# Kernel tuning notes

Measured on AMD Instinct MI355X. Metric: run time of the kernel, lower is better.

The kernel has to match this reference:

```python
import jax, jax.numpy as jnp
import numpy as np

H = 16          # num_heads
DH = 128        # head_dim
TILE = 128      # tile_size
TOPK = 8        # top_k_tiles
NEG = -1e10


def _rotate_half(x):
    half = x.shape[-1] // 2
    return jnp.concatenate([-x[..., half:], x[..., :half]], axis=-1)


def setup_inputs() -> dict:
    key = jax.random.key(0)
    B, S, D = 2, 2048, H * DH
    ks = jax.random.split(key, 5)
    x = jax.random.normal(ks[0], (B, S, D), dtype=jnp.float32)
    scale = 0.02
    wq = jax.random.normal(ks[1], (D, H * DH), dtype=jnp.float32) * scale
    wk = jax.random.normal(ks[2], (D, H * DH), dtype=jnp.float32) * scale
    wv = jax.random.normal(ks[3], (D, H * DH), dtype=jnp.float32) * scale
    wo = jax.random.normal(ks[4], (H * DH, D), dtype=jnp.float32) * scale
    # RoPE tables: freqs_cis.real / .imag, shape [S, head_dim//2]
    inv_freq = 1.0 / (10000.0 ** (np.arange(0, DH, 2, dtype=np.float32) / DH))
    angles = np.arange(S, dtype=np.float32)[:, None] * inv_freq[None, :]
    cos = jnp.asarray(np.cos(angles), dtype=jnp.float32)
    sin = jnp.asarray(np.sin(angles), dtype=jnp.float32)
    return {"x": x, "wq": wq, "wk": wk, "wv": wv, "wo": wo, "cos": cos, "sin": sin}


def reference(x, wq, wk, wv, wo, cos, sin):
    B, S, D = x.shape
    # QKV projections -> [B, H, S, Dh]
    q = (x @ wq).reshape(B, S, H, DH).transpose(0, 2, 1, 3)
    k = (x @ wk).reshape(B, S, H, DH).transpose(0, 2, 1, 3)
    v = (x @ wv).reshape(B, S, H, DH).transpose(0, 2, 1, 3)
    # RoPE (half-split / rotate_half form), in fp32 as in source
    cf = jnp.concatenate([cos, cos], axis=-1)[None, None].astype(jnp.float32)  # [1,1,S,Dh]
    sf = jnp.concatenate([sin, sin], axis=-1)[None, None].astype(jnp.float32)
    q = q.astype(jnp.float32)
    k = k.astype(jnp.float32)
    q = q * cf + _rotate_half(q) * sf
    k = k * cf + _rotate_half(k) * sf
    # Full causal logits [B,H,S,S] (short-seq branch: seq_len <= 8192)
    scale = 1.0 / jnp.sqrt(jnp.float32(DH))
    logits = jnp.einsum('bhqd,bhkd->bhqk', q, k) * scale
    causal = jnp.tril(jnp.ones((S, S), dtype=bool))
    logits = jnp.where(causal[None, None], logits, NEG)
    # Tile scoring: softmax over representative rows, tile max-pool, top-k tiles
    num_tiles = S // TILE
    rep_pos = jnp.arange(TILE - 1, S, TILE)           # last query of each tile
    rep_w = jax.nn.softmax(logits[:, :, rep_pos, :], axis=-1)  # [B,H,nt,S]
    tile_scores = jnp.max(rep_w.reshape(B, H, num_tiles, num_tiles, TILE), axis=-1)
    _, group_tile_indices = jax.lax.top_k(tile_scores, min(TOPK, num_tiles))  # [B,H,nt,topk]
    # Full causal attention (explicit path, same math as dot_product_attention is_causal)
    weights = jax.nn.softmax(logits, axis=-1)
    out = jnp.einsum('bhqk,bhkd->bhqd', weights, v)
    out = out.transpose(0, 2, 1, 3).reshape(B, S, H * DH)
    out = out @ wo
    return out, group_tile_indices
```

## Files before the change

kernel.cpp:

```cpp
#include <hip/hip_runtime.h>
#include <cstdint>
#include <cstddef>


#define S_LEN 2048
#define NH 16
#define DHD 128
#define DMODEL 2048
#define MROWS 4096
#define SCALE 0.08838834764831845f
#define NEG10 -1e10f

typedef short short8 __attribute__((ext_vector_type(8)));
typedef __bf16 bf16x8 __attribute__((ext_vector_type(8)));
typedef float f32x4 __attribute__((ext_vector_type(4)));

#define MFMA16(a, b, c) __builtin_amdgcn_mfma_f32_16x16x32_bf16((a), (b), (c), 0, 0, 0)

__device__ __forceinline__ void gl16(const void* g, void* s) {
  __builtin_amdgcn_global_load_lds(
      (const __attribute__((address_space(1))) void*)g,
      (__attribute__((address_space(3))) void*)s, 16, 0, 0);
}

__device__ __forceinline__ unsigned short f2bf(float f) {
  unsigned u = __float_as_uint(f);
  return (unsigned short)((u + 0x7fffu + ((u >> 16) & 1u)) >> 16);
}
__device__ __forceinline__ float bf2f(unsigned short h) {
  return __uint_as_float(((unsigned)h) << 16);
}

__global__ __launch_bounds__(256) void k_split_x(const float* __restrict__ x,
                                                 unsigned short* __restrict__ xh,
                                                 unsigned short* __restrict__ xl, int n4) {
  int i = blockIdx.x * blockDim.x + threadIdx.x;
  for (; i < n4; i += gridDim.x * blockDim.x) {
    float4 v = ((const float4*)x)[i];
    float f[4] = {v.x, v.y, v.z, v.w};
    unsigned short hh[4], ll[4];
#pragma unroll
    for (int j = 0; j < 4; j++) {
      hh[j] = f2bf(f[j]);
      ll[j] = f2bf(f[j] - bf2f(hh[j]));
    }
    ((ushort4*)xh)[i] = make_ushort4(hh[0], hh[1], hh[2], hh[3]);
    ((ushort4*)xl)[i] = make_ushort4(ll[0], ll[1], ll[2], ll[3]);
  }
}

template <int LO>
__global__ __launch_bounds__(256) void k_transw(const float* __restrict__ w,
                                                unsigned short* __restrict__ th,
                                                unsigned short* __restrict__ tl) {
  int n = blockIdx.x * 256 + threadIdx.x;
  int r0 = blockIdx.y * 32;
  float vals[32];
#pragma unroll
  for (int j = 0; j < 32; j++) vals[j] = w[(size_t)(r0 + j) * DMODEL + n];
  unsigned short hs[32];
#pragma unroll
  for (int j = 0; j < 32; j++) hs[j] = f2bf(vals[j]);
  unsigned short* dsth = th + (size_t)n * DMODEL + r0;
#pragma unroll
  for (int c = 0; c < 4; c++) {
    short8 v;
#pragma unroll
    for (int j = 0; j < 8; j++) v[j] = (short)hs[c * 8 + j];
    *(short8*)(dsth + c * 8) = v;
  }
  if (LO) {
    unsigned short ls[32];
#pragma unroll
    for (int j = 0; j < 32; j++) ls[j] = f2bf(vals[j] - bf2f(hs[j]));
    unsigned short* dstl = tl + (size_t)n * DMODEL + r0;
#pragma unroll
    for (int c = 0; c < 4; c++) {
      short8 v;
#pragma unroll
      for (int j = 0; j < 8; j++) v[j] = (short)ls[c * 8 + j];
      *(short8*)(dstl + c * 8) = v;
    }
  }
}

template <int SPLIT, int EPI>
__global__ __launch_bounds__(256) void k_gemm(const unsigned short* __restrict__ A,
                                              const unsigned short* __restrict__ Al,
                                              const unsigned short* __restrict__ Bt,
                                              const unsigned short* __restrict__ Btl,
                                              void* __restrict__ outp) {
  constexpr int NSM = (SPLIT ? 4 : 2) * 4096;
  __shared__ unsigned short sm[NSM];
  unsigned short* sAh = sm;
  unsigned short* sAl = SPLIT ? (sm + 4096) : nullptr;
  unsigned short* sBh = sm + (SPLIT ? 8192 : 4096);
  unsigned short* sBl = SPLIT ? (sm + 12288) : nullptr;

  const int tid = threadIdx.x;
  const int l = tid & 63, w = tid >> 6;
  const int lr = l & 15, lk = l >> 4;
  const int rowBase = blockIdx.y * 128;
  const int colBase = blockIdx.x * 128;
  const int wr = (w >> 1) * 64, wc = (w & 1) * 64;

  f32x4 zero = {0.f, 0.f, 0.f, 0.f};
  f32x4 acc[4][4];
#pragma unroll
  for (int mi = 0; mi < 4; mi++)
#pragma unroll
    for (int ni = 0; ni < 4; ni++) acc[mi][ni] = zero;

  for (int kt = 0; kt < 64; ++kt) {
#pragma unroll
    for (int p = 0; p < 2; ++p) {
      int c = w * 128 + p * 64 + l;
      int row = c >> 2, sl = c & 3;
      int kbl = sl ^ ((row >> 1) & 3);
      size_t srca = (size_t)(rowBase + row) * DMODEL + kt * 32 + kbl * 8;
      gl16(A + srca, (char*)sAh + c * 16);
      if (SPLIT) gl16(Al + srca, (char*)sAl + c * 16);
      size_t srcb = (size_t)(colBase + row) * DMODEL + kt * 32 + kbl * 8;
      gl16(Bt + srcb, (char*)sBh + c * 16);
      if (SPLIT) gl16(Btl + srcb, (char*)sBl + c * 16);
    }
    __syncthreads();

    bf16x8 ah[4], alo[4], bh[4], blo[4];
#pragma unroll
    for (int mi = 0; mi < 4; mi++) {
      int row = wr + mi * 16 + lr;
      int off = row * 32 + ((lk ^ ((row >> 1) & 3)) * 8);
      ah[mi] = *(const bf16x8*)(sAh + off);
      if (SPLIT) alo[mi] = *(const bf16x8*)(sAl + off);
    }
#pragma unroll
    for (int ni = 0; ni < 4; ni++) {
      int row = wc + ni * 16 + lr;
      int off = row * 32 + ((lk ^ ((row >> 1) & 3)) * 8);
      bh[ni] = *(const bf16x8*)(sBh + off);
      if (SPLIT) blo[ni] = *(const bf16x8*)(sBl + off);
    }
#pragma unroll
    for (int mi = 0; mi < 4; mi++)
#pragma unroll
      for (int ni = 0; ni < 4; ni++) {
        acc[mi][ni] = MFMA16(ah[mi], bh[ni], acc[mi][ni]);
        if (SPLIT) {
          acc[mi][ni] = MFMA16(alo[mi], bh[ni], acc[mi][ni]);
          acc[mi][ni] = MFMA16(ah[mi], blo[ni], acc[mi][ni]);
        }
      }
    __syncthreads();
  }

#pragma unroll
  for (int mi = 0; mi < 4; mi++)
#pragma unroll
    for (int ni = 0; ni < 4; ni++)
#pragma unroll
      for (int r = 0; r < 4; r++) {
        int row = rowBase + wr + mi * 16 + lk * 4 + r;
        int col = colBase + wc + ni * 16 + lr;
        float v = acc[mi][ni][r];
        if (EPI == 2) {
          ((float*)outp)[(size_t)row * DMODEL + col] = v;
        } else {
          size_t idx = (((size_t)(row >> 11) * NH + (col >> 7)) * S_LEN + (row & 2047)) * DHD +
                       (col & 127);
          if (EPI == 1)
            ((float*)outp)[idx] = v;
          else
            ((unsigned short*)outp)[idx] = f2bf(v);
        }
      }
}

__global__ __launch_bounds__(256) void k_rope_q(unsigned short* __restrict__ q,
                                                const float* __restrict__ cosT,
                                                const float* __restrict__ sinT) {
  int t = blockIdx.x * blockDim.x + threadIdx.x;
  int row = t >> 4;
  int i4 = (t & 15) * 4;
  int s = row & 2047;
  unsigned short* p0 = q + (size_t)row * DHD + i4;
  unsigned short* p1 = p0 + 64;
  ushort4 a = *(ushort4*)p0, b = *(ushort4*)p1;
  float4 c = *(const float4*)(cosT + (size_t)s * 64 + i4);
  float4 sn = *(const float4*)(sinT + (size_t)s * 64 + i4);
  float av[4] = {bf2f(a.x), bf2f(a.y), bf2f(a.z), bf2f(a.w)};
  float bv[4] = {bf2f(b.x), bf2f(b.y), bf2f(b.z), bf2f(b.w)};
  float cv[4] = {c.x, c.y, c.z, c.w}, sv[4] = {sn.x, sn.y, sn.z, sn.w};
  unsigned short na[4], nb[4];
#pragma unroll
  for (int j = 0; j < 4; j++) {
    na[j] = f2bf(av[j] * cv[j] - bv[j] * sv[j]);
    nb[j] = f2bf(bv[j] * cv[j] + av[j] * sv[j]);
  }
  *(ushort4*)p0 = make_ushort4(na[0], na[1], na[2], na[3]);
  *(ushort4*)p1 = make_ushort4(nb[0], nb[1], nb[2], nb[3]);
}

__global__ __launch_bounds__(256) void k_rope_k(float* __restrict__ kf,
                                                unsigned short* __restrict__ kb,
                                                const float* __restrict__ cosT,
                                                const float* __restrict__ sinT) {
  int t = blockIdx.x * blockDim.x + threadIdx.x;
  int row = t >> 4;
  int i4 = (t & 15) * 4;
  int s = row & 2047;
  float* p0 = kf + (size_t)row * DHD + i4;
  float* p1 = p0 + 64;
  float4 a = *(float4*)p0, b = *(float4*)p1;
  float4 c = *(const float4*)(cosT + (size_t)s * 64 + i4);
  float4 sn = *(const float4*)(sinT + (size_t)s * 64 + i4);
  float av[4] = {a.x, a.y, a.z, a.w}, bv[4] = {b.x, b.y, b.z, b.w};
  float cv[4] = {c.x, c.y, c.z, c.w}, sv[4] = {sn.x, sn.y, sn.z, sn.w};
  float na[4], nb[4];
#pragma unroll
  for (int j = 0; j < 4; j++) {
    na[j] = av[j] * cv[j] - bv[j] * sv[j];
    nb[j] = bv[j] * cv[j] + av[j] * sv[j];
  }
  *(float4*)p0 = make_float4(na[0], na[1], na[2], na[3]);
  *(float4*)p1 = make_float4(nb[0], nb[1], nb[2], nb[3]);
  unsigned short* kb0 = kb + (size_t)row * DHD + i4;
  *(ushort4*)kb0 = make_ushort4(f2bf(na[0]), f2bf(na[1]), f2bf(na[2]), f2bf(na[3]));
  *(ushort4*)(kb0 + 64) = make_ushort4(f2bf(nb[0]), f2bf(nb[1]), f2bf(nb[2]), f2bf(nb[3]));
}

__global__ __launch_bounds__(256) void k_vtrans(const unsigned short* __restrict__ v,
                                                unsigned short* __restrict__ vt) {
  int bh = blockIdx.y;
  int s0 = blockIdx.x * 64 + (threadIdx.x >> 7) * 32;
  int d = threadIdx.x & 127;
  unsigned short tmp[32];
#pragma unroll
  for (int j = 0; j < 32; j++) tmp[j] = v[((size_t)bh * S_LEN + s0 + j) * DHD + d];
  unsigned short* dst = vt + ((size_t)bh * DHD + d) * S_LEN + s0;
#pragma unroll
  for (int c = 0; c < 4; c++) {
    short8 x;
#pragma unroll
    for (int j = 0; j < 8; j++) x[j] = (short)tmp[c * 8 + j];
    *(short8*)(dst + c * 8) = x;
  }
}

__global__ __launch_bounds__(256) void k_attn(const unsigned short* __restrict__ q,
                                              const unsigned short* __restrict__ k,
                                              const unsigned short* __restrict__ vt,
                                              unsigned short* __restrict__ o) {
  __shared__ unsigned short sK[64 * 128];
  __shared__ unsigned short sV[128 * 64];
  __shared__ unsigned short sP[128 * 72];
  const int qt = blockIdx.x, bh = blockIdx.y;
  const int b = bh >> 4, h = bh & 15;
  const int tid = threadIdx.x, l = tid & 63, w = tid >> 6;
  const int lr = l & 15, lk = l >> 4;
  const int q0 = qt * 128;
  const size_t kvbase = (size_t)bh * S_LEN * DHD;

  bf16x8 qf[2][4];
#pragma unroll
  for (int mi = 0; mi < 2; mi++)
#pragma unroll
    for (int kd = 0; kd < 4; kd++) {
      int row = q0 + w * 32 + mi * 16 + lr;
      qf[mi][kd] = *(const bf16x8*)(q + kvbase + (size_t)row * DHD + kd * 32 + lk * 8);
    }

  f32x4 zero = {0.f, 0.f, 0.f, 0.f};
  f32x4 acc[2][8];
#pragma unroll
  for (int mi = 0; mi < 2; mi++)
#pragma unroll
    for (int ni = 0; ni < 8; ni++) acc[mi][ni] = zero;
  float mrow[2][4], lsum[2][4];
#pragma unroll
  for (int mi = 0; mi < 2; mi++)
#pragma unroll
    for (int r = 0; r < 4; r++) {
      mrow[mi][r] = -3e38f;
      lsum[mi][r] = 0.f;
    }

  const int nkt = 2 * qt + 2;
  for (int kt = 0; kt < nkt; ++kt) {
#pragma unroll
    for (int p = 0; p < 4; ++p) {
      int c = p * 256 + w * 64 + l;
      int kp = c >> 4, sl = c & 15;
      int sls = sl ^ (kp & 7);
      gl16(k + kvbase + (size_t)(kt * 64 + kp) * DHD + sls * 8, (char*)sK + c * 16);
    }
#pragma unroll
    for (int p = 0; p < 4; ++p) {
      int c = p * 256 + w * 64 + l;
      int dh = c >> 3, sl = c & 7;
      int sls = sl ^ (dh & 7);
      gl16(vt + ((size_t)bh * DHD + dh) * S_LEN + kt * 64 + sls * 8, (char*)sV + c * 16);
    }
    __syncthreads();

    f32x4 sf[2][4];
#pragma unroll
    for (int mi = 0; mi < 2; mi++)
#pragma unroll
      for (int nk = 0; nk < 4; nk++) {
        f32x4 sacc = zero;
#pragma unroll
        for (int kd = 0; kd < 4; kd++) {
          int row = nk * 16 + lr;
          int off = row * 128 + (((kd * 4 + lk) ^ (row & 7)) * 8);
          bf16x8 kf = *(const bf16x8*)(sK + off);
          sacc = MFMA16(qf[mi][kd], kf, sacc);
        }
        sf[mi][nk] = sacc;
      }

#pragma unroll
    for (int mi = 0; mi < 2; mi++) {
#pragma unroll
      for (int r = 0; r < 4; r++) {
        int qpos = q0 + w * 32 + mi * 16 + lk * 4 + r;
        float lg[4];
        float mx = -3e38f;
#pragma unroll
        for (int nk = 0; nk < 4; nk++) {
          int kpos = kt * 64 + nk * 16 + lr;
          float vsc = sf[mi][nk][r] * SCALE;
          if (kpos > qpos) vsc = -3e38f;
          lg[nk] = vsc;
          mx = fmaxf(mx, vsc);
        }
#pragma unroll
        for (int d = 1; d < 16; d <<= 1) mx = fmaxf(mx, __shfl_xor(mx, d));
        float mnew = fmaxf(mrow[mi][r], mx);
        float corr = expf(mrow[mi][r] - mnew);
        float ps = 0.f;
        unsigned short pb[4];
#pragma unroll
        for (int nk = 0; nk < 4; nk++) {
          float p = expf(lg[nk] - mnew);
          ps += p;
          pb[nk] = f2bf(p);
        }
#pragma unroll
        for (int d = 1; d < 16; d <<= 1) ps += __shfl_xor(ps, d);
        lsum[mi][r] = lsum[mi][r] * corr + ps;
        mrow[mi][r] = mnew;
#pragma unroll
        for (int ni = 0; ni < 8; ni++) acc[mi][ni][r] *= corr;
        int prow = w * 32 + mi * 16 + lk * 4 + r;
#pragma unroll
        for (int nk = 0; nk < 4; nk++) sP[prow * 72 + nk * 16 + lr] = pb[nk];
      }
    }
    __syncthreads();

    bf16x8 pa[2][2];
#pragma unroll
    for (int mi = 0; mi < 2; mi++)
#pragma unroll
      for (int ks = 0; ks < 2; ks++) {
        int row = w * 32 + mi * 16 + lr;
        pa[mi][ks] = *(const bf16x8*)(sP + row * 72 + ks * 32 + lk * 8);
      }
#pragma unroll
    for (int ni = 0; ni < 8; ni++) {
#pragma unroll
      for (int ks = 0; ks < 2; ks++) {
        int row = ni * 16 + lr;
        int off = row * 64 + (((ks * 4 + lk) ^ (row & 7)) * 8);
        bf16x8 vf = *(const bf16x8*)(sV + off);
#pragma unroll
        for (int mi = 0; mi < 2; mi++) acc[mi][ni] = MFMA16(pa[mi][ks], vf, acc[mi][ni]);
      }
    }
    __syncthreads();
  }

#pragma unroll
  for (int mi = 0; mi < 2; mi++)
#pragma unroll
    for (int r = 0; r < 4; r++) {
      float inv = 1.0f / lsum[mi][r];
      int srow = q0 + w * 32 + mi * 16 + lk * 4 + r;
      size_t base = ((size_t)b * S_LEN + srow) * DMODEL + h * DHD;
#pragma unroll
      for (int ni = 0; ni < 8; ni++) o[base + ni * 16 + lr] = f2bf(acc[mi][ni][r] * inv);
    }
}

__global__ __launch_bounds__(256) void k_score(const float* __restrict__ x,
                                               const float* __restrict__ wq,
                                               const float* __restrict__ cosT,
                                               const float* __restrict__ sinT,
                                               const float* __restrict__ kf,
                                               float* __restrict__ idxout) {
  const int t = blockIdx.x, bh = blockIdx.y;
  const int b = bh >> 4, h = bh & 15;
  const int srep = t * 128 + 127;
  const int tid = threadIdx.x;
  __shared__ float qr[128];
  __shared__ float part[256];
  __shared__ unsigned keys[16];

  {
    const int dh = tid & 127, half = tid >> 7;
    const float* xrow = x + ((size_t)b * S_LEN + srep) * DMODEL;
    const float* wcol = wq + (size_t)h * DHD + dh;
    float s0 = 0.f, s1 = 0.f, s2 = 0.f, s3 = 0.f;
    const int dbase = half * 1024;
    for (int d = 0; d < 1024; d += 4) {
      int dd = dbase + d;
      s0 = fmaf(xrow[dd], wcol[(size_t)dd * DMODEL], s0);
      s1 = fmaf(xrow[dd + 1], wcol[(size_t)(dd + 1) * DMODEL], s1);
      s2 = fmaf(xrow[dd + 2], wcol[(size_t)(dd + 2) * DMODEL], s2);
      s3 = fmaf(xrow[dd + 3], wcol[(size_t)(dd + 3) * DMODEL], s3);
    }
    part[tid] = (s0 + s1) + (s2 + s3);
  }
  if (tid < 16) keys[tid] = ~__float_as_uint(NEG10);
  __syncthreads();
  if (tid < 64) {
    int i = tid;
    float q0v = part[i] + part[i + 128];
    float q1v = part[i + 64] + part[i + 192];
    float c = cosT[(size_t)srep * 64 + i], sn = sinT[(size_t)srep * 64 + i];
    qr[i] = q0v * c - q1v * sn;
    qr[i + 64] = q1v * c + q0v * sn;
  }
  __syncthreads();

  for (int j = tid; j <= srep; j += 256) {
    const float4* krow = (const float4*)(kf + ((size_t)bh * S_LEN + j) * DHD);
    float a0 = 0.f, a1 = 0.f, a2 = 0.f, a3 = 0.f;
#pragma unroll 8
    for (int d4 = 0; d4 < 32; d4++) {
      float4 kv = krow[d4];
      const float* qq = qr + d4 * 4;
      a0 = fmaf(kv.x, qq[0], a0);
      a1 = fmaf(kv.y, qq[1], a1);
      a2 = fmaf(kv.z, qq[2], a2);
      a3 = fmaf(kv.w, qq[3], a3);
    }
    float lg = ((a0 + a1) + (a2 + a3)) * SCALE;
    unsigned u = __float_as_uint(lg);
    unsigned key = (u & 0x80000000u) ? ~u : (u | 0x80000000u);
    atomicMax(&keys[j >> 7], key);
  }
  __syncthreads();

  if (tid == 0) {
    unsigned used = 0;
    float* dst = idxout + ((size_t)bh * 16 + t) * 8;
    for (int r = 0; r < 8; ++r) {
      int best = -1;
      unsigned bk = 0;
#pragma unroll
      for (int tl = 0; tl < 16; ++tl) {
        if (used & (1u << tl)) continue;
        unsigned kv = keys[tl];
        if (best < 0 || kv > bk) {
          bk = kv;
          best = tl;
        }
      }
      used |= (1u << best);
      dst[r] = (float)best;
    }
  }
}

extern "C" void kernel_launch(void* const* d_in, const int* in_sizes, int n_in,
                              void* d_out, int out_size, void* d_ws, size_t ws_size,
                              hipStream_t stream) {
  (void)in_sizes; (void)n_in; (void)out_size; (void)ws_size;
  const float* x = (const float*)d_in[0];
  const float* wq = (const float*)d_in[1];
  const float* wk = (const float*)d_in[2];
  const float* wv = (const float*)d_in[3];
  const float* wo = (const float*)d_in[4];
  const float* cosT = (const float*)d_in[5];
  const float* sinT = (const float*)d_in[6];
  float* out0 = (float*)d_out;
  float* out1 = out0 + (size_t)MROWS * DMODEL;
  float* kf32 = out0;

  char* ws = (char*)d_ws;
  size_t off = 0;
  auto alloc = [&](size_t bytes) {
    void* p = ws + off;
    off += (bytes + 255) & ~(size_t)255;
    return p;
  };
  unsigned short* xh = (unsigned short*)alloc(16777216);
  unsigned short* xl = (unsigned short*)alloc(16777216);
  unsigned short* wqT = (unsigned short*)alloc(8388608);
  unsigned short* wkT = (unsigned short*)alloc(8388608);
  unsigned short* wkTl = (unsigned short*)alloc(8388608);
  unsigned short* wvT = (unsigned short*)alloc(8388608);
  unsigned short* woT = (unsigned short*)alloc(8388608);
  unsigned short* qbf = (unsigned short*)alloc(16777216);
  unsigned short* kbf = (unsigned short*)alloc(16777216);
  unsigned short* vbf = (unsigned short*)alloc(16777216);
  unsigned short* obf = xh;
  unsigned short* vtbf = xl;

  k_split_x<<<2048, 256, 0, stream>>>(x, xh, xl, MROWS * DMODEL / 4);
  dim3 gtw(8, 64);
  k_transw<0><<<gtw, 256, 0, stream>>>(wq, wqT, nullptr);
  k_transw<1><<<gtw, 256, 0, stream>>>(wk, wkT, wkTl);
  k_transw<0><<<gtw, 256, 0, stream>>>(wv, wvT, nullptr);
  k_transw<0><<<gtw, 256, 0, stream>>>(wo, woT, nullptr);

  dim3 gg(16, 32);
  k_gemm<0, 0><<<gg, 256, 0, stream>>>(xh, nullptr, wqT, nullptr, qbf);
  k_gemm<1, 1><<<gg, 256, 0, stream>>>(xh, xl, wkT, wkTl, kf32);
  k_gemm<0, 0><<<gg, 256, 0, stream>>>(xh, nullptr, wvT, nullptr, vbf);

  k_rope_q<<<4096, 256, 0, stream>>>(qbf, cosT, sinT);
  k_rope_k<<<4096, 256, 0, stream>>>(kf32, kbf, cosT, sinT);

  k_vtrans<<<dim3(32, 32), 256, 0, stream>>>(vbf, vtbf);
  k_attn<<<dim3(16, 32), 256, 0, stream>>>(qbf, kbf, vtbf, obf);

  k_score<<<dim3(16, 32), 256, 0, stream>>>(x, wq, cosT, sinT, kf32, out1);

  k_gemm<0, 2><<<gg, 256, 0, stream>>>(obf, nullptr, woT, nullptr, out0);
}
```

Baseline: 781.6 us.

## Shrink attention query tile to 64 rows and use exp2 softmax

The attention kernel now gives each block 64 query rows instead of 128, so each wave handles 16 rows and the grid doubles to 32x32 blocks. Causal masking is applied only on the diagonal key tile, and the softmax folds log2(e) into the scale so it can use exp2f. The aim is more blocks and higher occupancy (launch bounds now request 3 blocks per CU) and less masking and exponent work. In exchange, each block reuses every K/V tile it loads across half as many queries, so total K/V traffic from global memory roughly doubles.

```diff
diff --git a/kernel.cpp b/kernel.cpp
--- a/kernel.cpp
+++ b/kernel.cpp
@@ -9,6 +9,7 @@
 #define DMODEL 2048
 #define MROWS 4096
 #define SCALE 0.08838834764831845f
+#define SCALE_L2E (0.08838834764831845f * 1.4426950408889634f)
 #define NEG10 -1e10f
 
 typedef short short8 __attribute__((ext_vector_type(8)));
@@ -247,126 +248,113 @@
   }
 }
 
-__global__ __launch_bounds__(256) void k_attn(const unsigned short* __restrict__ q,
-                                              const unsigned short* __restrict__ k,
-                                              const unsigned short* __restrict__ vt,
-                                              unsigned short* __restrict__ o) {
+__global__ __launch_bounds__(256, 3) void k_attn(const unsigned short* __restrict__ q,
+                                                 const unsigned short* __restrict__ k,
+                                                 const unsigned short* __restrict__ vt,
+                                                 unsigned short* __restrict__ o) {
   __shared__ unsigned short sK[64 * 128];
   __shared__ unsigned short sV[128 * 64];
-  __shared__ unsigned short sP[128 * 72];
+  __shared__ unsigned short sP[64 * 72];
   const int qt = blockIdx.x, bh = blockIdx.y;
   const int b = bh >> 4, h = bh & 15;
   const int tid = threadIdx.x, l = tid & 63, w = tid >> 6;
   const int lr = l & 15, lk = l >> 4;
-  const int q0 = qt * 128;
+  const int q0 = qt * 64;
   const size_t kvbase = (size_t)bh * S_LEN * DHD;
 
-  bf16x8 qf[2][4];
-#pragma unroll
-  for (int mi = 0; mi < 2; mi++)
-#pragma unroll
-    for (int kd = 0; kd < 4; kd++) {
-      int row = q0 + w * 32 + mi * 16 + lr;
-      qf[mi][kd] = *(const bf16x8*)(q + kvbase + (size_t)row * DHD + kd * 32 + lk * 8);
-    }
+  bf16x8 qf[4];
+#pragma unroll
+  for (int kd = 0; kd < 4; kd++) {
+    int row = q0 + w * 16 + lr;
+    qf[kd] = *(const bf16x8*)(q + kvbase + (size_t)row * DHD + kd * 32 + lk * 8);
+  }
 
   f32x4 zero = {0.f, 0.f, 0.f, 0.f};
-  f32x4 acc[2][8];
-#pragma unroll
-  for (int mi = 0; mi < 2; mi++)
-#pragma unroll
-    for (int ni = 0; ni < 8; ni++) acc[mi][ni] = zero;
-  float mrow[2][4], lsum[2][4];
-#pragma unroll
-  for (int mi = 0; mi < 2; mi++)
-#pragma unroll
-    for (int r = 0; r < 4; r++) {
-      mrow[mi][r] = -3e38f;
-      lsum[mi][r] = 0.f;
-    }
-
-  const int nkt = 2 * qt + 2;
-  for (int kt = 0; kt < nkt; ++kt) {
+  f32x4 acc[8];
+#pragma unroll
+  for (int ni = 0; ni < 8; ni++) acc[ni] = zero;
+  float mrow[4], lsum[4];
+#pragma unroll
+  for (int r = 0; r < 4; r++) {
+    mrow[r] = -1e38f;
+    lsum[r] = 0.f;
+  }
+
+  for (int kt = 0; kt <= qt; ++kt) {
 #pragma unroll
     for (int p = 0; p < 4; ++p) {
-      int c = p * 256 + w * 64 + l;
+      int c = p * 256 + tid;
       int kp = c >> 4, sl = c & 15;
       int sls = sl ^ (kp & 7);
       gl16(k + kvbase + (size_t)(kt * 64 + kp) * DHD + sls * 8, (char*)sK + c * 16);
     }
 #pragma unroll
     for (int p = 0; p < 4; ++p) {
-      int c = p * 256 + w * 64 + l;
+      int c = p * 256 + tid;
       int dh = c >> 3, sl = c & 7;
       int sls = sl ^ (dh & 7);
       gl16(vt + ((size_t)bh * DHD + dh) * S_LEN + kt * 64 + sls * 8, (char*)sV + c * 16);
     }
     __syncthreads();
 
-    f32x4 sf[2][4];
-#pragma unroll
-    for (int mi = 0; mi < 2; mi++)
+    f32x4 sf[4];
+#pragma unroll
+    for (int nk = 0; nk < 4; nk++) {
+      f32x4 sacc = zero;
+#pragma unroll
+      for (int kd = 0; kd < 4; kd++) {
+        int row = nk * 16 + lr;
+        int off = row * 128 + (((kd * 4 + lk) ^ (row & 7)) * 8);
+        bf16x8 kfrag = *(const bf16x8*)(sK + off);
+        sacc = MFMA16(qf[kd], kfrag, sacc);
+      }
+      sf[nk] = sacc;
+    }
+
+    const bool diag = (kt == qt);
+#pragma unroll
+    for (int r = 0; r < 4; r++) {
+      int qpos = q0 + w * 16 + lk * 4 + r;
+      float lg[4];
+      float mx = -3e38f;
 #pragma unroll
       for (int nk = 0; nk < 4; nk++) {
-        f32x4 sacc = zero;
-#pragma unroll
-        for (int kd = 0; kd < 4; kd++) {
-          int row = nk * 16 + lr;
-          int off = row * 128 + (((kd * 4 + lk) ^ (row & 7)) * 8);
-          bf16x8 kf = *(const bf16x8*)(sK + off);
-          sacc = MFMA16(qf[mi][kd], kf, sacc);
-        }
-        sf[mi][nk] = sacc;
-      }
-
-#pragma unroll
-    for (int mi = 0; mi < 2; mi++) {
-#pragma unroll
-      for (int r = 0; r < 4; r++) {
-        int qpos = q0 + w * 32 + mi * 16 + lk * 4 + r;
-        float lg[4];
-        float mx = -3e38f;
-#pragma unroll
-        for (int nk = 0; nk < 4; nk++) {
-          int kpos = kt * 64 + nk * 16 + lr;
-          float vsc = sf[mi][nk][r] * SCALE;
-          if (kpos > qpos) vsc = -3e38f;
-          lg[nk] = vsc;
-          mx = fmaxf(mx, vsc);
-        }
-#pragma unroll
-        for (int d = 1; d < 16; d <<= 1) mx = fmaxf(mx, __shfl_xor(mx, d));
-        float mnew = fmaxf(mrow[mi][r], mx);
-        float corr = expf(mrow[mi][r] - mnew);
-        float ps = 0.f;
-        unsigned short pb[4];
-#pragma unroll
-        for (int nk = 0; nk < 4; nk++) {
-          float p = expf(lg[nk] - mnew);
-          ps += p;
-          pb[nk] = f2bf(p);
-        }
-#pragma unroll
-        for (int d = 1; d < 16; d <<= 1) ps += __shfl_xor(ps, d);
-        lsum[mi][r] = lsum[mi][r] * corr + ps;
-        mrow[mi][r] = mnew;
-#pragma unroll
-        for (int ni = 0; ni < 8; ni++) acc[mi][ni][r] *= corr;
-        int prow = w * 32 + mi * 16 + lk * 4 + r;
-#pragma unroll
-        for (int nk = 0; nk < 4; nk++) sP[prow * 72 + nk * 16 + lr] = pb[nk];
-      }
+        int kpos = kt * 64 + nk * 16 + lr;
+        float vsc = sf[nk][r] * SCALE_L2E;
+        if (diag && kpos > qpos) vsc = -3e38f;
+        lg[nk] = vsc;
+        mx = fmaxf(mx, vsc);
+      }
+#pragma unroll
+      for (int d = 1; d < 16; d <<= 1) mx = fmaxf(mx, __shfl_xor(mx, d));
+      float mnew = fmaxf(mrow[r], mx);
+      float corr = exp2f(mrow[r] - mnew);
+      float ps = 0.f;
+      unsigned short pb[4];
+#pragma unroll
+      for (int nk = 0; nk < 4; nk++) {
+        float p = exp2f(lg[nk] - mnew);
+        ps += p;
+        pb[nk] = f2bf(p);
+      }
+#pragma unroll
+      for (int d = 1; d < 16; d <<= 1) ps += __shfl_xor(ps, d);
+      lsum[r] = lsum[r] * corr + ps;
+      mrow[r] = mnew;
+#pragma unroll
+      for (int ni = 0; ni < 8; ni++) acc[ni][r] *= corr;
+      int prow = w * 16 + lk * 4 + r;
+#pragma unroll
+      for (int nk = 0; nk < 4; nk++) sP[prow * 72 + nk * 16 + lr] = pb[nk];
     }
     __syncthreads();
 
-    bf16x8 pa[2][2];
-#pragma unroll
-    for (int mi = 0; mi < 2; mi++)
-#pragma unroll
-      for (int ks = 0; ks < 2; ks++) {
-        int row = w * 32 + mi * 16 + lr;
-        pa[mi][ks] = *(const bf16x8*)(sP + row * 72 + ks * 32 + lk * 8);
-      }
+    bf16x8 pa[2];
+#pragma unroll
+    for (int ks = 0; ks < 2; ks++) {
+      int row = w * 16 + lr;
+      pa[ks] = *(const bf16x8*)(sP + row * 72 + ks * 32 + lk * 8);
+    }
 #pragma unroll
     for (int ni = 0; ni < 8; ni++) {
 #pragma unroll
@@ -374,23 +362,20 @@
         int row = ni * 16 + lr;
         int off = row * 64 + (((ks * 4 + lk) ^ (row & 7)) * 8);
         bf16x8 vf = *(const bf16x8*)(sV + off);
-#pragma unroll
-        for (int mi = 0; mi < 2; mi++) acc[mi][ni] = MFMA16(pa[mi][ks], vf, acc[mi][ni]);
+        acc[ni] = MFMA16(pa[ks], vf, acc[ni]);
       }
     }
     __syncthreads();
   }
 
 #pragma unroll
-  for (int mi = 0; mi < 2; mi++)
-#pragma unroll
-    for (int r = 0; r < 4; r++) {
-      float inv = 1.0f / lsum[mi][r];
-      int srow = q0 + w * 32 + mi * 16 + lk * 4 + r;
-      size_t base = ((size_t)b * S_LEN + srow) * DMODEL + h * DHD;
-#pragma unroll
-      for (int ni = 0; ni < 8; ni++) o[base + ni * 16 + lr] = f2bf(acc[mi][ni][r] * inv);
-    }
+  for (int r = 0; r < 4; r++) {
+    float inv = 1.0f / lsum[r];
+    int srow = q0 + w * 16 + lk * 4 + r;
+    size_t base = ((size_t)b * S_LEN + srow) * DMODEL + h * DHD;
+#pragma unroll
+    for (int ni = 0; ni < 8; ni++) o[base + ni * 16 + lr] = f2bf(acc[ni][r] * inv);
+  }
 }
 
 __global__ __launch_bounds__(256) void k_score(const float* __restrict__ x,
@@ -525,7 +510,7 @@
   k_rope_k<<<4096, 256, 0, stream>>>(kf32, kbf, cosT, sinT);
 
   k_vtrans<<<dim3(32, 32), 256, 0, stream>>>(vbf, vtbf);
-  k_attn<<<dim3(16, 32), 256, 0, stream>>>(qbf, kbf, vtbf, obf);
+  k_attn<<<dim3(32, 32), 256, 0, stream>>>(qbf, kbf, vtbf, obf);
 
   k_score<<<dim3(16, 32), 256, 0, stream>>>(x, wq, cosT, sinT, kf32, out1);
 
```

Result: faster. 700.4 us (-10.4%).
